# Kernel optimization log

Hardware: AMD Instinct MI355X
Metric: run time of the kernel (lower is better)

The kernel has to match this reference:

```python
import jax, jax.numpy as jnp
import numpy as np

NEG_INF = -1e9


def setup_inputs() -> dict:
    key = jax.random.key(0)
    k1, k2, k3 = jax.random.split(key, 3)
    B, N, F_IN, F_OUT = 8, 4096, 128, 64
    h = jax.random.normal(k1, (B, N, F_IN), dtype=jnp.float32)
    # xavier_uniform with gain=1.414 on [F_IN, F_OUT]
    limit = 1.414 * np.sqrt(6.0 / (F_IN + F_OUT))
    W = jax.random.uniform(k2, (F_IN, F_OUT), dtype=jnp.float32, minval=-limit, maxval=limit)
    adj = jax.random.randint(k3, (N, N), 0, 2, dtype=jnp.int32)
    return {"h": h, "W": W, "adj": adj}


def reference(h, W, adj):
    # h: [B, N, F_in], W: [F_in, F_out], adj: [N, N]
    F_out = W.shape[1]
    Wh = jnp.einsum('bnf,fo->bno', h, W)                      # [B, N, F_out]
    scores = jnp.einsum('bnd,bmd->bnm', Wh, Wh) / np.sqrt(F_out).astype(np.float32)
    attention = jnp.where(adj[None, :, :] > 0, scores, NEG_INF)
    attention = jax.nn.softmax(attention, axis=2)             # [B, N, N]
    # dropout p=0.0 / eval mode -> identity
    h_prime = jnp.einsum('bnm,bmd->bnd', attention, Wh)       # [B, N, F_out]
    return jax.nn.elu(h_prime)  # concat=True path
```

## Files before the change

### kernel.cpp

```cpp
#include <hip/hip_runtime.h>

typedef _Float16 half8  __attribute__((ext_vector_type(8)));
typedef _Float16 half4v __attribute__((ext_vector_type(4)));
typedef float    float4v __attribute__((ext_vector_type(4)));

#define N_ 4096
#define B_ 8
#define D_ 64
#define F_ 128

__global__ __launch_bounds__(256) void pack_adj_kernel(const int* __restrict__ adj,
                                                       unsigned long long* __restrict__ bits) {
  int i = blockIdx.x * 256 + threadIdx.x;
  unsigned long long m = __ballot(adj[i] > 0);
  if ((threadIdx.x & 63) == 0) bits[i >> 6] = m;
}

__global__ __launch_bounds__(256) void wh_kernel(const float* __restrict__ h,
                                                 const float* __restrict__ W,
                                                 _Float16* __restrict__ Wh16) {
  __shared__ __align__(16) float    hs[64][132];
  __shared__ __align__(16) _Float16 wt[64][132];
  const int t = threadIdx.x;
  const int rowbase = blockIdx.x * 64;
  const float4v* hg = (const float4v*)(h + (size_t)rowbase * F_);
#pragma unroll
  for (int k = 0; k < 8; ++k) {
    int i4 = t + k * 256;
    float4v v = hg[i4];
    int r = i4 >> 5, c4 = (i4 & 31) * 4;
    *(float4v*)&hs[r][c4] = v;
  }
#pragma unroll
  for (int k = 0; k < 8; ++k) {
    int i4 = t + k * 256;
    float4v v = ((const float4v*)W)[i4];
    int f = i4 >> 4, c4 = (i4 & 15) * 4;
    wt[c4 + 0][f] = (_Float16)v[0];
    wt[c4 + 1][f] = (_Float16)v[1];
    wt[c4 + 2][f] = (_Float16)v[2];
    wt[c4 + 3][f] = (_Float16)v[3];
  }
  __syncthreads();
  const int w = t >> 6, lane = t & 63;
  const int r0 = w * 16;
  float acc[16];
#pragma unroll
  for (int i = 0; i < 16; ++i) acc[i] = 0.f;
#pragma unroll 4
  for (int f4 = 0; f4 < 32; ++f4) {
    half4v wv = *(half4v*)&wt[lane][f4 * 4];
    float w0 = (float)wv[0], w1 = (float)wv[1], w2 = (float)wv[2], w3 = (float)wv[3];
#pragma unroll
    for (int i = 0; i < 16; ++i) {
      float4v hv = *(float4v*)&hs[r0 + i][f4 * 4];
      acc[i] += hv[0] * w0 + hv[1] * w1 + hv[2] * w2 + hv[3] * w3;
    }
  }
#pragma unroll
  for (int i = 0; i < 16; ++i)
    Wh16[(size_t)(rowbase + r0 + i) * D_ + lane] = (_Float16)acc[i];
}

__global__ __launch_bounds__(256) void tr_kernel(const _Float16* __restrict__ Wh16,
                                                 _Float16* __restrict__ WhT16) {
  __shared__ __align__(16) _Float16 tl[64][72];
  int bid = blockIdx.x;
  int b  = bid >> 6;
  int kb = (bid & 63) * 64;
  int t  = threadIdx.x;
  int kl = t >> 2, c0 = (t & 3) * 16;
  const _Float16* src = Wh16 + ((size_t)(b * N_ + kb + kl)) * D_ + c0;
  *(half8*)&tl[kl][c0]     = *(const half8*)src;
  *(half8*)&tl[kl][c0 + 8] = *(const half8*)(src + 8);
  __syncthreads();
  int dl = t >> 2, k0 = (t & 3) * 16;
  half8 o0, o1;
#pragma unroll
  for (int i = 0; i < 8; ++i) o0[i] = tl[k0 + i][dl];
#pragma unroll
  for (int i = 0; i < 8; ++i) o1[i] = tl[k0 + 8 + i][dl];
  _Float16* dst = WhT16 + ((size_t)(b * D_ + dl)) * N_ + kb + k0;
  *(half8*)dst       = o0;
  *(half8*)(dst + 8) = o1;
}

__global__ __launch_bounds__(512, 4) void attn_kernel(
    const unsigned long long* __restrict__ bits,
    const _Float16* __restrict__ Wh,
    const _Float16* __restrict__ WhT,
    float* __restrict__ out) {
  __shared__ __align__(16) char lds[49152];
  const int tid  = threadIdx.x;
  const int w    = tid >> 6;
  const int lane = tid & 63;
  const int g    = lane >> 4;
  const int c    = lane & 15;
  const int qi   = w & 3;
  const int s    = w >> 2;
  const int bid  = blockIdx.x;
  const int b    = bid >> 6;
  const int q0b  = (bid & 63) * 64;
  const int q0w  = q0b + qi * 16;

  const _Float16* Whb  = Wh  + (size_t)b * N_ * D_;
  const _Float16* WhTb = WhT + (size_t)b * D_ * N_;
  _Float16* Kst = (_Float16*)(lds + s * 8192);
  _Float16* Vst = (_Float16*)(lds + 16384 + s * 8192);
  char* Pb = lds + 32768 + w * 2048;

  const int e0  = (qi * 2 + 0) * 64 + lane;
  const int e1  = (qi * 2 + 1) * 64 + lane;
  const int r0e = e0 >> 3, s0e = (e0 & 7) ^ (r0e & 7);
  const int r1e = e1 >> 3, s1e = (e1 & 7) ^ (r1e & 7);

  half8 qf[2];
#pragma unroll
  for (int ds = 0; ds < 2; ++ds) {
    half8 v = *(const half8*)(Whb + (size_t)(q0w + c) * D_ + ds * 32 + g * 8);
    qf[ds] = v * (_Float16)0.125f;
  }

  float4v o_acc[4];
#pragma unroll
  for (int d = 0; d < 4; ++d) o_acc[d] = (float4v){0.f, 0.f, 0.f, 0.f};
  float mrow = -1e30f, lrow = 0.f;

  const unsigned long long* bq = bits + (size_t)(q0w + c) * 64 + s * 32;

  int k0n = (s * 32) * 64;
  half8 ka = *(const half8*)(Whb + (size_t)(k0n + r0e) * D_ + s0e * 8);
  half8 kb = *(const half8*)(Whb + (size_t)(k0n + r1e) * D_ + s1e * 8);
  half8 va = *(const half8*)(WhTb + (size_t)r0e * N_ + k0n + s0e * 8);
  half8 vb = *(const half8*)(WhTb + (size_t)r1e * N_ + k0n + s1e * 8);
  unsigned long long bw = bq[0];

  for (int t = 0; t < 32; ++t) {
    __syncthreads();
    *(half8*)(Kst + e0 * 8) = ka;
    *(half8*)(Kst + e1 * 8) = kb;
    *(half8*)(Vst + e0 * 8) = va;
    *(half8*)(Vst + e1 * 8) = vb;
    __syncthreads();

    const int t1 = (t + 1 < 32) ? t + 1 : 31;
    k0n = (s * 32 + t1) * 64;
    ka = *(const half8*)(Whb + (size_t)(k0n + r0e) * D_ + s0e * 8);
    kb = *(const half8*)(Whb + (size_t)(k0n + r1e) * D_ + s1e * 8);
    va = *(const half8*)(WhTb + (size_t)r0e * N_ + k0n + s0e * 8);
    vb = *(const half8*)(WhTb + (size_t)r1e * N_ + k0n + s1e * 8);
    unsigned long long bwn = bq[t1];

    float4v sac[4];
#pragma unroll
    for (int st = 0; st < 4; ++st) {
      const _Float16* kr = Kst + (st * 16 + c) * 64;
      half8 kf0 = *(const half8*)(kr + ((g       ^ (c & 7)) * 8));
      half8 kf1 = *(const half8*)(kr + (((g + 4) ^ (c & 7)) * 8));
      float4v z = (float4v){0.f, 0.f, 0.f, 0.f};
      z = __builtin_amdgcn_mfma_f32_16x16x32_f16(kf0, qf[0], z, 0, 0, 0);
      z = __builtin_amdgcn_mfma_f32_16x16x32_f16(kf1, qf[1], z, 0, 0, 0);
      sac[st] = z;
    }

    float tmax = -1e30f;
#pragma unroll
    for (int st = 0; st < 4; ++st) {
      unsigned wb = (unsigned)(bw >> (st * 16 + g * 4));
#pragma unroll
      for (int j = 0; j < 4; ++j) {
        float v = (wb & (1u << j)) ? sac[st][j] : -1e9f;
        sac[st][j] = v;
        tmax = fmaxf(tmax, v);
      }
    }
    tmax = fmaxf(tmax, __shfl_xor(tmax, 16));
    tmax = fmaxf(tmax, __shfl_xor(tmax, 32));

    float mnew  = fmaxf(mrow, tmax);
    float alpha = __expf(mrow - mnew);
    mrow = mnew;
    lrow *= alpha;
#pragma unroll
    for (int j = 0; j < 4; ++j) {
      float aj = __shfl(alpha, (lane & 48) | (g * 4 + j));
#pragma unroll
      for (int d = 0; d < 4; ++d) o_acc[d][j] *= aj;
    }

#pragma unroll
    for (int st = 0; st < 4; ++st) {
      float p0 = __expf(sac[st][0] - mrow);
      float p1 = __expf(sac[st][1] - mrow);
      float p2 = __expf(sac[st][2] - mrow);
      float p3 = __expf(sac[st][3] - mrow);
      lrow += (p0 + p1) + (p2 + p3);
      uint2 pr;
      pr.x = __builtin_bit_cast(unsigned, __builtin_amdgcn_cvt_pkrtz(p0, p1));
      pr.y = __builtin_bit_cast(unsigned, __builtin_amdgcn_cvt_pkrtz(p2, p3));
      const int cell = st * 2 + (g >> 1);
      *(uint2*)(Pb + (cell * 16 + c) * 16 + (g & 1) * 8) = pr;
    }

#pragma unroll
    for (int ks = 0; ks < 2; ++ks) {
      half8 af = *(const half8*)(Pb + ((ks * 4 + g) * 16 + c) * 16);
#pragma unroll
      for (int d = 0; d < 4; ++d) {
        const int vrow = d * 16 + c;
        half8 vf = *(const half8*)(Vst + vrow * 64 + (((ks * 4 + g) ^ (c & 7)) * 8));
        o_acc[d] = __builtin_amdgcn_mfma_f32_16x16x32_f16(af, vf, o_acc[d], 0, 0, 0);
      }
    }
    bw = bwn;
  }

  lrow += __shfl_xor(lrow, 16);
  lrow += __shfl_xor(lrow, 32);
  __syncthreads();
  float* Ob = (float*)lds;
#pragma unroll
  for (int d = 0; d < 4; ++d)
#pragma unroll
    for (int j = 0; j < 4; ++j)
      Ob[(w * 16 + g * 4 + j) * 66 + d * 16 + c] = o_acc[d][j];
  float2* mlb = (float2*)(lds + 36864);
  if (g == 0) mlb[w * 16 + c] = make_float2(mrow, lrow);
  __syncthreads();

#pragma unroll
  for (int it = 0; it < 8; ++it) {
    int r   = w + it * 8;
    int col = lane;
    int qq = r >> 4, rl = r & 15;
    float2 ml0 = mlb[qq * 16 + rl];
    float2 ml1 = mlb[(qq + 4) * 16 + rl];
    float mm = fmaxf(ml0.x, ml1.x);
    float a0 = __expf(ml0.x - mm);
    float a1 = __expf(ml1.x - mm);
    float l  = a0 * ml0.y + a1 * ml1.y;
    float o  = a0 * Ob[(qq * 16 + rl) * 66 + col] + a1 * Ob[((qq + 4) * 16 + rl) * 66 + col];
    float x  = o / l;
    x = x > 0.f ? x : (__expf(x) - 1.f);
    out[((size_t)b * N_ + q0b + r) * D_ + col] = x;
  }
}

extern "C" void kernel_launch(void* const* d_in, const int* in_sizes, int n_in,
                              void* d_out, int out_size, void* d_ws, size_t ws_size,
                              hipStream_t stream) {
  const float* h = (const float*)d_in[0];
  const float* W = (const float*)d_in[1];
  const int* adj = (const int*)d_in[2];
  float* out = (float*)d_out;

  char* ws = (char*)d_ws;
  unsigned long long* bits = (unsigned long long*)ws;
  _Float16* Wh16  = (_Float16*)(ws + (2u << 20));
  _Float16* WhT16 = (_Float16*)(ws + (6u << 20));

  hipLaunchKernelGGL(pack_adj_kernel, dim3((N_ * N_) / 256), dim3(256), 0, stream, adj, bits);
  hipLaunchKernelGGL(wh_kernel,   dim3((B_ * N_) / 64), dim3(256), 0, stream, h, W, Wh16);
  hipLaunchKernelGGL(tr_kernel,   dim3(B_ * (N_ / 64)), dim3(256), 0, stream, Wh16, WhT16);
  hipLaunchKernelGGL(attn_kernel, dim3(B_ * (N_ / 64)), dim3(512), 0, stream, bits, Wh16, WhT16, out);
}
```

Baseline: 212.3 us.

## Vectorize adjacency packing, fuse transpose into Wh, double-buffer K/V, use exp2

The adjacency packer now reads int4 vectors and assembles 64-bit masks from per-thread nibbles in shared memory. This replaces one ballot per element and cuts the block count by a factor of four. The transpose kernel is folded into the Wh projection kernel, which removes one launch and one re-read of Wh. The attention loop double-buffers the K/V tiles in LDS so there is one barrier per iteration instead of two, and it uses exp2 with log2(e) folded into the query scale. This doubles LDS use, which may lower occupancy below the four blocks per CU requested in the launch bounds.

```diff
diff --git a/kernel.cpp b/kernel.cpp
--- a/kernel.cpp
+++ b/kernel.cpp
@@ -9,18 +9,31 @@
 #define D_ 64
 #define F_ 128
 
-__global__ __launch_bounds__(256) void pack_adj_kernel(const int* __restrict__ adj,
+__global__ __launch_bounds__(256) void pack_adj_kernel(const int4* __restrict__ adj4,
                                                        unsigned long long* __restrict__ bits) {
-  int i = blockIdx.x * 256 + threadIdx.x;
-  unsigned long long m = __ballot(adj[i] > 0);
-  if ((threadIdx.x & 63) == 0) bits[i >> 6] = m;
+  __shared__ unsigned char nib[256];
+  const int t = threadIdx.x;
+  int4 v = adj4[(size_t)blockIdx.x * 256 + t];
+  unsigned n = (v.x > 0 ? 1u : 0u) | (v.y > 0 ? 2u : 0u) |
+               (v.z > 0 ? 4u : 0u) | (v.w > 0 ? 8u : 0u);
+  nib[t] = (unsigned char)n;
+  __syncthreads();
+  if (t < 16) {
+    const unsigned char* p = &nib[t * 16];
+    unsigned long long wv = 0;
+#pragma unroll
+    for (int i = 0; i < 16; ++i) wv |= (unsigned long long)p[i] << (4 * i);
+    bits[(size_t)blockIdx.x * 16 + t] = wv;
+  }
 }
 
 __global__ __launch_bounds__(256) void wh_kernel(const float* __restrict__ h,
                                                  const float* __restrict__ W,
-                                                 _Float16* __restrict__ Wh16) {
+                                                 _Float16* __restrict__ Wh16,
+                                                 _Float16* __restrict__ WhT16) {
   __shared__ __align__(16) float    hs[64][132];
   __shared__ __align__(16) _Float16 wt[64][132];
+  __shared__ __align__(16) _Float16 otile[64][72];
   const int t = threadIdx.x;
   const int rowbase = blockIdx.x * 64;
   const float4v* hg = (const float4v*)(h + (size_t)rowbase * F_);
@@ -58,29 +71,20 @@
     }
   }
 #pragma unroll
-  for (int i = 0; i < 16; ++i)
-    Wh16[(size_t)(rowbase + r0 + i) * D_ + lane] = (_Float16)acc[i];
-}
-
-__global__ __launch_bounds__(256) void tr_kernel(const _Float16* __restrict__ Wh16,
-                                                 _Float16* __restrict__ WhT16) {
-  __shared__ __align__(16) _Float16 tl[64][72];
-  int bid = blockIdx.x;
-  int b  = bid >> 6;
-  int kb = (bid & 63) * 64;
-  int t  = threadIdx.x;
-  int kl = t >> 2, c0 = (t & 3) * 16;
-  const _Float16* src = Wh16 + ((size_t)(b * N_ + kb + kl)) * D_ + c0;
-  *(half8*)&tl[kl][c0]     = *(const half8*)src;
-  *(half8*)&tl[kl][c0 + 8] = *(const half8*)(src + 8);
-  __syncthreads();
-  int dl = t >> 2, k0 = (t & 3) * 16;
+  for (int i = 0; i < 16; ++i) {
+    _Float16 hv = (_Float16)acc[i];
+    Wh16[(size_t)(rowbase + r0 + i) * D_ + lane] = hv;
+    otile[r0 + i][lane] = hv;
+  }
+  __syncthreads();
+  const int dl = t >> 2, k0t = (t & 3) * 16;
   half8 o0, o1;
 #pragma unroll
-  for (int i = 0; i < 8; ++i) o0[i] = tl[k0 + i][dl];
-#pragma unroll
-  for (int i = 0; i < 8; ++i) o1[i] = tl[k0 + 8 + i][dl];
-  _Float16* dst = WhT16 + ((size_t)(b * D_ + dl)) * N_ + kb + k0;
+  for (int i = 0; i < 8; ++i) o0[i] = otile[k0t + i][dl];
+#pragma unroll
+  for (int i = 0; i < 8; ++i) o1[i] = otile[k0t + 8 + i][dl];
+  const int b = rowbase >> 12, n0 = rowbase & 4095;
+  _Float16* dst = WhT16 + ((size_t)(b * D_ + dl)) * N_ + n0 + k0t;
   *(half8*)dst       = o0;
   *(half8*)(dst + 8) = o1;
 }
@@ -90,7 +94,7 @@
     const _Float16* __restrict__ Wh,
     const _Float16* __restrict__ WhT,
     float* __restrict__ out) {
-  __shared__ __align__(16) char lds[49152];
+  __shared__ __align__(16) char lds[81920];
   const int tid  = threadIdx.x;
   const int w    = tid >> 6;
   const int lane = tid & 63;
@@ -105,9 +109,9 @@
 
   const _Float16* Whb  = Wh  + (size_t)b * N_ * D_;
   const _Float16* WhTb = WhT + (size_t)b * D_ * N_;
-  _Float16* Kst = (_Float16*)(lds + s * 8192);
-  _Float16* Vst = (_Float16*)(lds + 16384 + s * 8192);
-  char* Pb = lds + 32768 + w * 2048;
+  char* Kbase = lds + s * 16384;
+  char* Vbase = lds + 32768 + s * 16384;
+  char* Pb    = lds + 65536 + w * 2048;
 
   const int e0  = (qi * 2 + 0) * 64 + lane;
   const int e1  = (qi * 2 + 1) * 64 + lane;
@@ -118,7 +122,7 @@
 #pragma unroll
   for (int ds = 0; ds < 2; ++ds) {
     half8 v = *(const half8*)(Whb + (size_t)(q0w + c) * D_ + ds * 32 + g * 8);
-    qf[ds] = v * (_Float16)0.125f;
+    qf[ds] = v * (_Float16)0.18033688f;
   }
 
   float4v o_acc[4];
@@ -134,14 +138,16 @@
   half8 va = *(const half8*)(WhTb + (size_t)r0e * N_ + k0n + s0e * 8);
   half8 vb = *(const half8*)(WhTb + (size_t)r1e * N_ + k0n + s1e * 8);
   unsigned long long bw = bq[0];
+  *(half8*)(Kbase + e0 * 16) = ka;
+  *(half8*)(Kbase + e1 * 16) = kb;
+  *(half8*)(Vbase + e0 * 16) = va;
+  *(half8*)(Vbase + e1 * 16) = vb;
+  __syncthreads();
 
   for (int t = 0; t < 32; ++t) {
-    __syncthreads();
-    *(half8*)(Kst + e0 * 8) = ka;
-    *(half8*)(Kst + e1 * 8) = kb;
-    *(half8*)(Vst + e0 * 8) = va;
-    *(half8*)(Vst + e1 * 8) = vb;
-    __syncthreads();
+    const int cur = (t & 1) * 8192, nxt = 8192 - cur;
+    const _Float16* Kc = (const _Float16*)(Kbase + cur);
+    const _Float16* Vc = (const _Float16*)(Vbase + cur);
 
     const int t1 = (t + 1 < 32) ? t + 1 : 31;
     k0n = (s * 32 + t1) * 64;
@@ -154,7 +160,7 @@
     float4v sac[4];
 #pragma unroll
     for (int st = 0; st < 4; ++st) {
-      const _Float16* kr = Kst + (st * 16 + c) * 64;
+      const _Float16* kr = Kc + (st * 16 + c) * 64;
       half8 kf0 = *(const half8*)(kr + ((g       ^ (c & 7)) * 8));
       half8 kf1 = *(const half8*)(kr + (((g + 4) ^ (c & 7)) * 8));
       float4v z = (float4v){0.f, 0.f, 0.f, 0.f};
@@ -178,7 +184,7 @@
     tmax = fmaxf(tmax, __shfl_xor(tmax, 32));
 
     float mnew  = fmaxf(mrow, tmax);
-    float alpha = __expf(mrow - mnew);
+    float alpha = exp2f(mrow - mnew);
     mrow = mnew;
     lrow *= alpha;
 #pragma unroll
@@ -190,10 +196,10 @@
 
 #pragma unroll
     for (int st = 0; st < 4; ++st) {
-      float p0 = __expf(sac[st][0] - mrow);
-      float p1 = __expf(sac[st][1] - mrow);
-      float p2 = __expf(sac[st][2] - mrow);
-      float p3 = __expf(sac[st][3] - mrow);
+      float p0 = exp2f(sac[st][0] - mrow);
+      float p1 = exp2f(sac[st][1] - mrow);
+      float p2 = exp2f(sac[st][2] - mrow);
+      float p3 = exp2f(sac[st][3] - mrow);
       lrow += (p0 + p1) + (p2 + p3);
       uint2 pr;
       pr.x = __builtin_bit_cast(unsigned, __builtin_amdgcn_cvt_pkrtz(p0, p1));
@@ -208,10 +214,16 @@
 #pragma unroll
       for (int d = 0; d < 4; ++d) {
         const int vrow = d * 16 + c;
-        half8 vf = *(const half8*)(Vst + vrow * 64 + (((ks * 4 + g) ^ (c & 7)) * 8));
+        half8 vf = *(const half8*)(Vc + vrow * 64 + (((ks * 4 + g) ^ (c & 7)) * 8));
         o_acc[d] = __builtin_amdgcn_mfma_f32_16x16x32_f16(af, vf, o_acc[d], 0, 0, 0);
       }
     }
+
+    *(half8*)(Kbase + nxt + e0 * 16) = ka;
+    *(half8*)(Kbase + nxt + e1 * 16) = kb;
+    *(half8*)(Vbase + nxt + e0 * 16) = va;
+    *(half8*)(Vbase + nxt + e1 * 16) = vb;
+    __syncthreads();
     bw = bwn;
   }
 
@@ -236,8 +248,8 @@
     float2 ml0 = mlb[qq * 16 + rl];
     float2 ml1 = mlb[(qq + 4) * 16 + rl];
     float mm = fmaxf(ml0.x, ml1.x);
-    float a0 = __expf(ml0.x - mm);
-    float a1 = __expf(ml1.x - mm);
+    float a0 = exp2f(ml0.x - mm);
+    float a1 = exp2f(ml1.x - mm);
     float l  = a0 * ml0.y + a1 * ml1.y;
     float o  = a0 * Ob[(qq * 16 + rl) * 66 + col] + a1 * Ob[((qq + 4) * 16 + rl) * 66 + col];
     float x  = o / l;
@@ -259,8 +271,8 @@
   _Float16* Wh16  = (_Float16*)(ws + (2u << 20));
   _Float16* WhT16 = (_Float16*)(ws + (6u << 20));
 
-  hipLaunchKernelGGL(pack_adj_kernel, dim3((N_ * N_) / 256), dim3(256), 0, stream, adj, bits);
-  hipLaunchKernelGGL(wh_kernel,   dim3((B_ * N_) / 64), dim3(256), 0, stream, h, W, Wh16);
-  hipLaunchKernelGGL(tr_kernel,   dim3(B_ * (N_ / 64)), dim3(256), 0, stream, Wh16, WhT16);
+  hipLaunchKernelGGL(pack_adj_kernel, dim3((N_ * N_) / 1024), dim3(256), 0, stream,
+                     (const int4*)adj, bits);
+  hipLaunchKernelGGL(wh_kernel,   dim3((B_ * N_) / 64), dim3(256), 0, stream, h, W, Wh16, WhT16);
   hipLaunchKernelGGL(attn_kernel, dim3(B_ * (N_ / 64)), dim3(512), 0, stream, bits, Wh16, WhT16, out);
 }
```

Measured after the change: 204.6 us. -3.6%, faster.
